# Performance work log

Measured on AMD Instinct MI355X. Metric: run time of the kernel, lower is better.

The kernel has to match this reference:

```python
import jax, jax.numpy as jnp
import numpy as np

N = 100000
E = 3200000
HEADS = 4
DH = 16  # per-head dim
IN = 300
OUT2 = 32
SLOPE = 0.2  # PyG GATConv leaky_relu negative slope


def setup_inputs() -> dict:
    key = jax.random.key(0)
    ks = jax.random.split(key, 10)
    x = jax.random.normal(ks[0], (N, IN), dtype=jnp.float32)
    edge_index = jax.random.randint(ks[1], (2, E), 0, N, dtype=jnp.int64)
    sec_order_edge_index = jax.random.randint(ks[2], (2, E), 0, N, dtype=jnp.int64)
    # GATConv(300, 16, heads=4) params
    W1 = jax.random.normal(ks[3], (IN, HEADS * DH), dtype=jnp.float32) * (1.0 / np.sqrt(IN))
    att_src = jax.random.normal(ks[4], (HEADS, DH), dtype=jnp.float32) * 0.1
    att_dst = jax.random.normal(ks[5], (HEADS, DH), dtype=jnp.float32) * 0.1
    b1 = jnp.zeros((HEADS * DH,), dtype=jnp.float32)
    # GCNConv(64, 32) params
    W2 = jax.random.normal(ks[6], (HEADS * DH, OUT2), dtype=jnp.float32) * (1.0 / np.sqrt(HEADS * DH))
    b2 = jnp.zeros((OUT2,), dtype=jnp.float32)
    return {"x": x, "W1": W1, "att_src": att_src, "att_dst": att_dst, "b1": b1,
            "W2": W2, "b2": b2, "edge_index": edge_index,
            "sec_order_edge_index": sec_order_edge_index}


def _add_self_loops(edge_index, n):
    loop = jnp.arange(n, dtype=edge_index.dtype)
    src = jnp.concatenate([edge_index[0], loop])
    dst = jnp.concatenate([edge_index[1], loop])
    return src, dst


def _gat(x, W1, att_src, att_dst, b1, edge_index):
    n = x.shape[0]
    src, dst = _add_self_loops(edge_index, n)
    h = (x @ W1).reshape(n, HEADS, DH)                    # [N,H,D]
    a_s = jnp.einsum('nhd,hd->nh', h, att_src)            # [N,H]
    a_d = jnp.einsum('nhd,hd->nh', h, att_dst)
    e = jax.nn.leaky_relu(a_s[src] + a_d[dst], SLOPE)     # [Et,H]
    # segment softmax over edges grouped by destination node
    m = jax.ops.segment_max(e, dst, num_segments=n)       # [N,H]
    ex = jnp.exp(e - m[dst])
    denom = jax.ops.segment_sum(ex, dst, num_segments=n)  # [N,H] (>0: self-loops)
    alpha = ex / denom[dst]                               # [Et,H]
    out = jax.ops.segment_sum(h[src] * alpha[:, :, None], dst, num_segments=n)
    return out.reshape(n, HEADS * DH) + b1


def _gcn(x, W2, b2, edge_index):
    n = x.shape[0]
    src, dst = _add_self_loops(edge_index, n)
    deg = jax.ops.segment_sum(jnp.ones_like(dst, dtype=x.dtype), dst, num_segments=n)
    dinv = jnp.where(deg > 0, jax.lax.rsqrt(deg), 0.0)
    norm = dinv[src] * dinv[dst]                          # [Et]
    h = x @ W2                                            # [N,32]
    out = jax.ops.segment_sum(h[src] * norm[:, None], dst, num_segments=n)
    return out + b2


def reference(x, W1, att_src, att_dst, b1, W2, b2, edge_index, sec_order_edge_index):
    x1 = jax.nn.relu(_gat(x, W1, att_src, att_dst, b1, edge_index))
    # F.dropout with training=False is identity (eval mode)
    return _gcn(x1, W2, b2, sec_order_edge_index)
```

## Files before the change

kernel.cpp:

```cpp
#include <hip/hip_runtime.h>
#include <hip/hip_fp16.h>

#define N_NODES 100000
#define N_EDGES 3200000
#define TOT_E   (N_EDGES + N_NODES)
#define HEADS   4
#define DH      16
#define IN_F    300
#define HID     64
#define OUT2    32
#define SLOPE   0.2f
#define NBK     512
#define GSZ     196
#define EBLK    4096
#define NBA     ((TOT_E + EBLK - 1) / EBLK)

typedef _Float16 f16x8 __attribute__((ext_vector_type(8)));
typedef float    f32x4 __attribute__((ext_vector_type(4)));

__global__ void k_wcvt(const float* __restrict__ W1, __half* __restrict__ BT16) {
    int idx = blockIdx.x * 256 + threadIdx.x;
    if (idx >= HID * 320) return;
    int n = idx / 320, k = idx - n * 320;
    BT16[idx] = (k < IN_F) ? __float2half(W1[(size_t)k * HID + n]) : __float2half(0.f);
}

#define G1_BM 128
#define G1_BK 64
#define G1_NS 5

__global__ __launch_bounds__(256) void k_gemm1(const float* __restrict__ x,
                                               const __half* __restrict__ BT16,
                                               const float* __restrict__ att_src,
                                               const float* __restrict__ att_dst,
                                               __half* __restrict__ h16,
                                               float* __restrict__ as_ad) {
    __shared__ _Float16 At[G1_BM][G1_BK];
    __shared__ _Float16 Bt[HID][G1_BK];
    const int t = threadIdx.x;
    const int lane = t & 63, w = t >> 6;
    const int lr = lane & 15, lg = lane >> 4;
    const int row0 = blockIdx.x * G1_BM;
    const int wrow = w * 32;

    int arow[4], auc[4];
    const float* axp[4];
#pragma unroll
    for (int m = 0; m < 4; m++) {
        int id = t + m * 256;
        arow[m] = id >> 3; auc[m] = id & 7;
        int gr = row0 + arow[m];
        gr = (gr < N_NODES) ? gr : (N_NODES - 1);
        axp[m] = x + (size_t)gr * IN_F + auc[m] * 8;
    }
    int bn[2], buc[2];
    const __half* bxp[2];
#pragma unroll
    for (int q = 0; q < 2; q++) {
        int id = t + q * 256;
        bn[q] = id >> 3; buc[q] = id & 7;
        bxp[q] = BT16 + bn[q] * (G1_BK * G1_NS) + buc[q] * 8;
    }

    float4 ar[4][2];
    uint4  br[2];

    auto loadS = [&](int kb) {
        if (kb + G1_BK <= IN_F) {
#pragma unroll
            for (int m = 0; m < 4; m++) {
                ar[m][0] = *(const float4*)(axp[m] + kb);
                ar[m][1] = *(const float4*)(axp[m] + kb + 4);
            }
        } else {
#pragma unroll
            for (int m = 0; m < 4; m++) {
                float v[8];
#pragma unroll
                for (int e = 0; e < 8; e++) {
                    int k = kb + auc[m] * 8 + e;
                    v[e] = (k < IN_F) ? axp[m][kb + e] : 0.f;
                }
                ar[m][0] = make_float4(v[0], v[1], v[2], v[3]);
                ar[m][1] = make_float4(v[4], v[5], v[6], v[7]);
            }
        }
#pragma unroll
        for (int q = 0; q < 2; q++) br[q] = *(const uint4*)(bxp[q] + kb);
    };

    auto writeS = [&]() {
#pragma unroll
        for (int m = 0; m < 4; m++) {
            f16x8 pk;
            pk[0] = (_Float16)ar[m][0].x; pk[1] = (_Float16)ar[m][0].y;
            pk[2] = (_Float16)ar[m][0].z; pk[3] = (_Float16)ar[m][0].w;
            pk[4] = (_Float16)ar[m][1].x; pk[5] = (_Float16)ar[m][1].y;
            pk[6] = (_Float16)ar[m][1].z; pk[7] = (_Float16)ar[m][1].w;
            *(f16x8*)&At[arow[m]][(auc[m] ^ (arow[m] & 7)) << 3] = pk;
        }
#pragma unroll
        for (int q = 0; q < 2; q++)
            *(uint4*)&Bt[bn[q]][(buc[q] ^ (bn[q] & 7)) << 3] = br[q];
    };

    f32x4 acc[2][4];
#pragma unroll
    for (int mt = 0; mt < 2; mt++)
#pragma unroll
        for (int nt = 0; nt < 4; nt++) acc[mt][nt] = (f32x4){0.f, 0.f, 0.f, 0.f};

    loadS(0);
    for (int s = 0; s < G1_NS; s++) {
        __syncthreads();
        writeS();
        if (s + 1 < G1_NS) loadS((s + 1) * G1_BK);
        __syncthreads();
#pragma unroll
        for (int ks = 0; ks < 2; ks++) {
            const int u = ks * 4 + lg;
            f16x8 af[2], bf[4];
#pragma unroll
            for (int mt = 0; mt < 2; mt++) {
                int r = wrow + mt * 16 + lr;
                af[mt] = *(const f16x8*)&At[r][(u ^ (r & 7)) << 3];
            }
#pragma unroll
            for (int nt = 0; nt < 4; nt++) {
                int n = nt * 16 + lr;
                bf[nt] = *(const f16x8*)&Bt[n][(u ^ (n & 7)) << 3];
            }
#pragma unroll
            for (int mt = 0; mt < 2; mt++)
#pragma unroll
                for (int nt = 0; nt < 4; nt++)
                    acc[mt][nt] = __builtin_amdgcn_mfma_f32_16x16x32_f16(
                        af[mt], bf[nt], acc[mt][nt], 0, 0, 0);
        }
    }

    float ws4[4], wd4[4];
#pragma unroll
    for (int nt = 0; nt < 4; nt++) {
        ws4[nt] = att_src[nt * DH + lr];
        wd4[nt] = att_dst[nt * DH + lr];
    }

#pragma unroll
    for (int mt = 0; mt < 2; mt++) {
#pragma unroll
        for (int rg = 0; rg < 4; rg++) {
            int gr = row0 + wrow + mt * 16 + lg * 4 + rg;
            float s_[4], d_[4];
#pragma unroll
            for (int nt = 0; nt < 4; nt++) {
                float v = (float)acc[mt][nt][rg];
                float vs = v * ws4[nt], vd = v * wd4[nt];
                vs += __shfl_xor(vs, 1, 64); vs += __shfl_xor(vs, 2, 64);
                vs += __shfl_xor(vs, 4, 64); vs += __shfl_xor(vs, 8, 64);
                vd += __shfl_xor(vd, 1, 64); vd += __shfl_xor(vd, 2, 64);
                vd += __shfl_xor(vd, 4, 64); vd += __shfl_xor(vd, 8, 64);
                s_[nt] = vs; d_[nt] = vd;
            }
            if (gr < N_NODES) {
#pragma unroll
                for (int nt = 0; nt < 4; nt++)
                    h16[(size_t)gr * HID + nt * 16 + lr] =
                        __float2half((float)acc[mt][nt][rg]);
                if (lr == 0) {
                    *(float4*)&as_ad[gr * 8] =
                        make_float4(s_[0], s_[1], s_[2], s_[3]);
                    *(float4*)&as_ad[gr * 8 + 4] =
                        make_float4(d_[0], d_[1], d_[2], d_[3]);
                }
            }
        }
    }
}

__global__ __launch_bounds__(512) void k_chist(const int* __restrict__ ei1,
                                               const int* __restrict__ ei2,
                                               int* __restrict__ ccnt) {
    __shared__ int hist[NBK];
    int b = blockIdx.x; const int* ei; int* cc;
    if (b < NBA) { ei = ei1; cc = ccnt; }
    else         { ei = ei2; cc = ccnt + NBK; b -= NBA; }
    int t = threadIdx.x;
    hist[t] = 0;
    __syncthreads();
    int e0 = b * EBLK;
#pragma unroll
    for (int i = 0; i < 8; i++) {
        int e = e0 + i * 512 + t;
        if (e < TOT_E) {
            int dst = (e < N_EDGES) ? ei[N_EDGES + e] : (e - N_EDGES);
            atomicAdd(&hist[(unsigned int)dst / GSZ], 1);
        }
    }
    __syncthreads();
    { int v = hist[t]; if (v) atomicAdd(&cc[t], v); }
}

__global__ __launch_bounds__(1024) void k_cscan(const int* __restrict__ ccnt,
                                                int* __restrict__ crp,
                                                int* __restrict__ ccur) {
    __shared__ int sc[1024];
    int t = threadIdx.x;
    int idx = t & (NBK - 1);
    int own = ccnt[t];
    sc[t] = own;
    __syncthreads();
    for (int off = 1; off < NBK; off <<= 1) {
        int v = (idx >= off) ? sc[t - off] : 0;
        __syncthreads();
        sc[t] += v;
        __syncthreads();
    }
    int ex = sc[t] - own;
    crp[t] = ex; ccur[t] = ex;
}

__global__ __launch_bounds__(512) void k_binA(const int* __restrict__ ei1,
                                              const int* __restrict__ ei2,
                                              int* __restrict__ ccur,
                                              unsigned int* __restrict__ tmp) {
    __shared__ int hist[NBK];
    __shared__ int base[NBK];
    int b = blockIdx.x; const int* ei; int loff;
    if (b < NBA) { ei = ei1; loff = 0; }
    else         { ei = ei2; loff = 1; b -= NBA; }
    int t = threadIdx.x;
    hist[t] = 0;
    __syncthreads();
    unsigned int pk[8]; int cb[8], rk[8];
    int e0 = b * EBLK;
#pragma unroll
    for (int i = 0; i < 8; i++) {
        int e = e0 + i * 512 + t;
        cb[i] = -1;
        if (e < TOT_E) {
            int src, dst;
            if (e < N_EDGES) { src = ei[e]; dst = ei[N_EDGES + e]; }
            else             { src = e - N_EDGES; dst = src; }
            unsigned int c   = (unsigned int)dst / GSZ;
            unsigned int dlo = (unsigned int)dst - c * GSZ;
            cb[i] = (int)c;
            pk[i] = (dlo << 17) | (unsigned int)src;
            rk[i] = atomicAdd(&hist[c], 1);
        }
    }
    __syncthreads();
    {
        int v = hist[t];
        base[t] = v ? atomicAdd(&ccur[loff * NBK + t], v) : 0;
    }
    __syncthreads();
    unsigned int* tp = tmp + (size_t)loff * TOT_E;
#pragma unroll
    for (int i = 0; i < 8; i++)
        if (cb[i] >= 0) tp[base[cb[i]] + rk[i]] = pk[i];
}

__global__ __launch_bounds__(256) void k_binB(const unsigned int* __restrict__ tmp,
                                              const int* __restrict__ crp,
                                              int* __restrict__ rowptr,
                                              int* __restrict__ srcs,
                                              float* __restrict__ dinv) {
    __shared__ int cnt[GSZ + 1];
    __shared__ int sc[256];
    __shared__ int cur[GSZ + 1];
    int blk = blockIdx.x;
    int l = blk >> 9, b = blk & (NBK - 1);
    int t = threadIdx.x;
    int nbeg = b * GSZ;
    int ncnt = min(GSZ, N_NODES - nbeg);
    const int* crpl = crp + l * NBK;
    int ebeg = crpl[b];
    int eend = (b < NBK - 1) ? crpl[b + 1] : TOT_E;
    const unsigned int* tp = tmp + (size_t)l * TOT_E;
    for (int i = t; i < GSZ + 1; i += 256) cnt[i] = 0;
    __syncthreads();
    for (int e = ebeg + t; e < eend; e += 256)
        atomicAdd(&cnt[tp[e] >> 17], 1);
    __syncthreads();
    sc[t] = (t < ncnt) ? cnt[t] : 0;
    __syncthreads();
    for (int off = 1; off < 256; off <<= 1) {
        int v = (t >= off) ? sc[t - off] : 0;
        __syncthreads();
        sc[t] += v;
        __syncthreads();
    }
    if (t < ncnt) {
        int c = cnt[t];
        int gpos = ebeg + sc[t] - c;
        rowptr[l * N_NODES + nbeg + t] = gpos;
        cur[t] = gpos;
        if (l == 1) dinv[nbeg + t] = rsqrtf((float)c);
    }
    __syncthreads();
    int* so = srcs + (size_t)l * TOT_E;
    for (int e = ebeg + t; e < eend; e += 256) {
        unsigned int p = tp[e];
        int pos = atomicAdd(&cur[p >> 17], 1);
        so[pos] = (int)(p & 0x1FFFF);
    }
}

__global__ __launch_bounds__(256) void k_gat(const __half* __restrict__ h16,
                                             const float* __restrict__ as_ad,
                                             const int* __restrict__ rowptr,
                                             const int* __restrict__ srcs,
                                             const float* __restrict__ b1,
                                             __half* __restrict__ x1h) {
    int w = (blockIdx.x * 256 + threadIdx.x) >> 6;
    if (w >= N_NODES) return;
    int lane = threadIdx.x & 63;
    int eidx = lane >> 3;
    int cl = lane & 7;
    int hd = cl >> 1;
    int c0 = cl * 8;
    float ad = as_ad[w * 8 + 4 + hd];
    int beg = rowptr[w];
    int end = (w == N_NODES - 1) ? TOT_E : rowptr[w + 1];
    float l = 0.f;
    float a0 = 0.f, a1 = 0.f, a2 = 0.f, a3 = 0.f;
    float a4 = 0.f, a5 = 0.f, a6 = 0.f, a7 = 0.f;
#pragma unroll 4
    for (int j = beg; j < end; j += 8) {
        int je = j + eidx;
        int s = __builtin_nontemporal_load(&srcs[min(je, end - 1)]);
        uint4 raw = *(const uint4*)&h16[(size_t)s * HID + c0];
        float e = as_ad[s * 8 + hd] + ad;
        e = fminf(fmaxf(e, SLOPE * e), 60.f);
        float p = (je < end) ? __expf(e) : 0.f;
        l += p;
        const __half2* hv = (const __half2*)&raw;
        float2 f0 = __half22float2(hv[0]);
        float2 f1 = __half22float2(hv[1]);
        float2 f2 = __half22float2(hv[2]);
        float2 f3 = __half22float2(hv[3]);
        a0 += p * f0.x; a1 += p * f0.y; a2 += p * f1.x; a3 += p * f1.y;
        a4 += p * f2.x; a5 += p * f2.y; a6 += p * f3.x; a7 += p * f3.y;
    }
    l  += __shfl_xor(l, 8, 64);  l  += __shfl_xor(l, 16, 64);  l  += __shfl_xor(l, 32, 64);
    a0 += __shfl_xor(a0, 8, 64); a0 += __shfl_xor(a0, 16, 64); a0 += __shfl_xor(a0, 32, 64);
    a1 += __shfl_xor(a1, 8, 64); a1 += __shfl_xor(a1, 16, 64); a1 += __shfl_xor(a1, 32, 64);
    a2 += __shfl_xor(a2, 8, 64); a2 += __shfl_xor(a2, 16, 64); a2 += __shfl_xor(a2, 32, 64);
    a3 += __shfl_xor(a3, 8, 64); a3 += __shfl_xor(a3, 16, 64); a3 += __shfl_xor(a3, 32, 64);
    a4 += __shfl_xor(a4, 8, 64); a4 += __shfl_xor(a4, 16, 64); a4 += __shfl_xor(a4, 32, 64);
    a5 += __shfl_xor(a5, 8, 64); a5 += __shfl_xor(a5, 16, 64); a5 += __shfl_xor(a5, 32, 64);
    a6 += __shfl_xor(a6, 8, 64); a6 += __shfl_xor(a6, 16, 64); a6 += __shfl_xor(a6, 32, 64);
    a7 += __shfl_xor(a7, 8, 64); a7 += __shfl_xor(a7, 16, 64); a7 += __shfl_xor(a7, 32, 64);
    if (eidx == 0) {
        float rl = 1.f / l;
        float4 b0 = *(const float4*)&b1[c0];
        float4 b4 = *(const float4*)&b1[c0 + 4];
        f16x8 o;
        o[0] = (_Float16)fmaxf(a0 * rl + b0.x, 0.f);
        o[1] = (_Float16)fmaxf(a1 * rl + b0.y, 0.f);
        o[2] = (_Float16)fmaxf(a2 * rl + b0.z, 0.f);
        o[3] = (_Float16)fmaxf(a3 * rl + b0.w, 0.f);
        o[4] = (_Float16)fmaxf(a4 * rl + b4.x, 0.f);
        o[5] = (_Float16)fmaxf(a5 * rl + b4.y, 0.f);
        o[6] = (_Float16)fmaxf(a6 * rl + b4.z, 0.f);
        o[7] = (_Float16)fmaxf(a7 * rl + b4.w, 0.f);
        *(f16x8*)&x1h[(size_t)w * HID + c0] = o;
    }
}

__global__ __launch_bounds__(256) void k_gemm2(const __half* __restrict__ x1h,
                                               const float* __restrict__ W2,
                                               const float* __restrict__ dinv,
                                               __half* __restrict__ h2s) {
    __shared__ float wl[HID * OUT2];
    __shared__ float xl[32][HID];
    int t = threadIdx.x;
    for (int i = t; i < HID * OUT2; i += 256) wl[i] = W2[i];
    int row0 = blockIdx.x * 32;
    {
        int rr = t >> 3, kk0 = (t & 7) * 8;
        uint4 raw = *(const uint4*)&x1h[(size_t)(row0 + rr) * HID + kk0];
        const __half2* hv = (const __half2*)&raw;
#pragma unroll
        for (int q = 0; q < 4; q++) {
            float2 f = __half22float2(hv[q]);
            xl[rr][kk0 + 2 * q] = f.x;
            xl[rr][kk0 + 2 * q + 1] = f.y;
        }
    }
    __syncthreads();
    int r0 = (t >> 5) * 4, c = t & 31;
    float ac0 = 0.f, ac1 = 0.f, ac2 = 0.f, ac3 = 0.f;
#pragma unroll 8
    for (int k = 0; k < HID; k++) {
        float wv = wl[k * OUT2 + c];
        ac0 += xl[r0 + 0][k] * wv;
        ac1 += xl[r0 + 1][k] * wv;
        ac2 += xl[r0 + 2][k] * wv;
        ac3 += xl[r0 + 3][k] * wv;
    }
    h2s[(size_t)(row0 + r0 + 0) * OUT2 + c] = __float2half(ac0 * dinv[row0 + r0 + 0]);
    h2s[(size_t)(row0 + r0 + 1) * OUT2 + c] = __float2half(ac1 * dinv[row0 + r0 + 1]);
    h2s[(size_t)(row0 + r0 + 2) * OUT2 + c] = __float2half(ac2 * dinv[row0 + r0 + 2]);
    h2s[(size_t)(row0 + r0 + 3) * OUT2 + c] = __float2half(ac3 * dinv[row0 + r0 + 3]);
}

__global__ __launch_bounds__(256) void k_gcn(const __half* __restrict__ h2s,
                                             const float* __restrict__ dinv,
                                             const int* __restrict__ rowptr,
                                             const int* __restrict__ srcs,
                                             const float* __restrict__ b2,
                                             float* __restrict__ out) {
    int w = (blockIdx.x * 256 + threadIdx.x) >> 6;
    if (w >= N_NODES) return;
    int lane = threadIdx.x & 63;
    int eidx = lane >> 2;
    int cq = lane & 3;
    int c0 = cq * 8;
    int beg = rowptr[w];
    int end = (w == N_NODES - 1) ? TOT_E : rowptr[w + 1];
    float a0 = 0.f, a1 = 0.f, a2 = 0.f, a3 = 0.f;
    float a4 = 0.f, a5 = 0.f, a6 = 0.f, a7 = 0.f;
#pragma unroll 4
    for (int j = beg; j < end; j += 16) {
        int je = j + eidx;
        int s = __builtin_nontemporal_load(&srcs[min(je, end - 1)]);
        uint4 raw = *(const uint4*)&h2s[(size_t)s * OUT2 + c0];
        if (je < end) {
            const __half2* hv = (const __half2*)&raw;
            float2 f0 = __half22float2(hv[0]);
            float2 f1 = __half22float2(hv[1]);
            float2 f2 = __half22float2(hv[2]);
            float2 f3 = __half22float2(hv[3]);
            a0 += f0.x; a1 += f0.y; a2 += f1.x; a3 += f1.y;
            a4 += f2.x; a5 += f2.y; a6 += f3.x; a7 += f3.y;
        }
    }
    a0 += __shfl_xor(a0, 4, 64); a0 += __shfl_xor(a0, 8, 64); a0 += __shfl_xor(a0, 16, 64); a0 += __shfl_xor(a0, 32, 64);
    a1 += __shfl_xor(a1, 4, 64); a1 += __shfl_xor(a1, 8, 64); a1 += __shfl_xor(a1, 16, 64); a1 += __shfl_xor(a1, 32, 64);
    a2 += __shfl_xor(a2, 4, 64); a2 += __shfl_xor(a2, 8, 64); a2 += __shfl_xor(a2, 16, 64); a2 += __shfl_xor(a2, 32, 64);
    a3 += __shfl_xor(a3, 4, 64); a3 += __shfl_xor(a3, 8, 64); a3 += __shfl_xor(a3, 16, 64); a3 += __shfl_xor(a3, 32, 64);
    a4 += __shfl_xor(a4, 4, 64); a4 += __shfl_xor(a4, 8, 64); a4 += __shfl_xor(a4, 16, 64); a4 += __shfl_xor(a4, 32, 64);
    a5 += __shfl_xor(a5, 4, 64); a5 += __shfl_xor(a5, 8, 64); a5 += __shfl_xor(a5, 16, 64); a5 += __shfl_xor(a5, 32, 64);
    a6 += __shfl_xor(a6, 4, 64); a6 += __shfl_xor(a6, 8, 64); a6 += __shfl_xor(a6, 16, 64); a6 += __shfl_xor(a6, 32, 64);
    a7 += __shfl_xor(a7, 4, 64); a7 += __shfl_xor(a7, 8, 64); a7 += __shfl_xor(a7, 16, 64); a7 += __shfl_xor(a7, 32, 64);
    if (eidx == 0) {
        float dv = dinv[w];
        float4 b0 = *(const float4*)&b2[c0];
        float4 b4 = *(const float4*)&b2[c0 + 4];
        float4 o0 = make_float4(a0 * dv + b0.x, a1 * dv + b0.y,
                                a2 * dv + b0.z, a3 * dv + b0.w);
        float4 o4 = make_float4(a4 * dv + b4.x, a5 * dv + b4.y,
                                a6 * dv + b4.z, a7 * dv + b4.w);
        *(float4*)&out[(size_t)w * OUT2 + c0] = o0;
        *(float4*)&out[(size_t)w * OUT2 + c0 + 4] = o4;
    }
}

static inline size_t align_up(size_t v, size_t a) { return (v + a - 1) & ~(a - 1); }

extern "C" void kernel_launch(void* const* d_in, const int* in_sizes, int n_in,
                              void* d_out, int out_size, void* d_ws, size_t ws_size,
                              hipStream_t stream) {
    const float* x       = (const float*)d_in[0];
    const float* W1      = (const float*)d_in[1];
    const float* att_src = (const float*)d_in[2];
    const float* att_dst = (const float*)d_in[3];
    const float* b1      = (const float*)d_in[4];
    const float* W2      = (const float*)d_in[5];
    const float* b2      = (const float*)d_in[6];
    const int*   ei1     = (const int*)d_in[7];
    const int*   ei2     = (const int*)d_in[8];
    float* out = (float*)d_out;

    char* p = (char*)d_ws;
    size_t off = 0;
    auto carve = [&](size_t bytes) { void* q = p + off; off = align_up(off + bytes, 256); return q; };
    __half* h16   = (__half*)carve((size_t)N_NODES * HID * 2);
    __half* x1h   = (__half*)carve((size_t)N_NODES * HID * 2);
    __half* h2s   = (__half*)carve((size_t)N_NODES * OUT2 * 2);
    float* as_ad  = (float*)carve((size_t)N_NODES * 8 * 4);
    float* dinv   = (float*)carve((size_t)N_NODES * 4);
    int* rowptr   = (int*)carve((size_t)2 * N_NODES * 4);
    int* srcs     = (int*)carve((size_t)2 * TOT_E * 4);
    unsigned int* tmp = (unsigned int*)carve((size_t)2 * TOT_E * 4);
    int* ccnt     = (int*)carve((size_t)2 * NBK * 4);
    int* crp      = (int*)carve((size_t)2 * NBK * 4);
    int* ccur     = (int*)carve((size_t)2 * NBK * 4);
    __half* BT16  = (__half*)carve((size_t)HID * 320 * 2);
    (void)ws_size; (void)in_sizes; (void)n_in; (void)out_size;

    hipMemsetAsync(ccnt, 0, (size_t)2 * NBK * 4, stream);

    k_wcvt<<<(HID * 320 + 255) / 256, 256, 0, stream>>>(W1, BT16);
    k_gemm1<<<(N_NODES + G1_BM - 1) / G1_BM, 256, 0, stream>>>(x, BT16, att_src, att_dst, h16, as_ad);

    k_chist<<<2 * NBA, 512, 0, stream>>>(ei1, ei2, ccnt);
    k_cscan<<<1, 1024, 0, stream>>>(ccnt, crp, ccur);
    k_binA<<<2 * NBA, 512, 0, stream>>>(ei1, ei2, ccur, tmp);
    k_binB<<<2 * NBK, 256, 0, stream>>>(tmp, crp, rowptr, srcs, dinv);

    k_gat<<<N_NODES / 4, 256, 0, stream>>>(h16, as_ad, rowptr, srcs, b1, x1h);

    k_gemm2<<<N_NODES / 32, 256, 0, stream>>>(x1h, W2, dinv, h2s);

    k_gcn<<<N_NODES / 4, 256, 0, stream>>>(h2s, dinv, rowptr + N_NODES, srcs + TOT_E, b2, out);
}
```

Baseline: 544.9 us.

## Halve GEMM1 row tile and stage outputs through LDS for coalesced stores

Shrinks the projection GEMM block tile from 128 to 64 rows, so each wave computes one 16-row MFMA tile and the grid has twice as many blocks. The epilogue now writes the accumulators to shared memory and reads them back per row and head, replacing the shuffle-based attention reductions and scattered 2-byte stores with vectorized 16-byte stores to h16. The attention logits are now computed from fp16-rounded values rather than fp32 accumulators, which slightly changes numerics. The smaller tile loads the weight matrix more times in total.

After: 543.5 us. About the same (-0.3%).

```diff
diff --git a/kernel.cpp b/kernel.cpp
--- a/kernel.cpp
+++ b/kernel.cpp
@@ -25,7 +25,7 @@
     BT16[idx] = (k < IN_F) ? __float2half(W1[(size_t)k * HID + n]) : __float2half(0.f);
 }
 
-#define G1_BM 128
+#define G1_BM 64
 #define G1_BK 64
 #define G1_NS 5
 
@@ -41,12 +41,12 @@
     const int lane = t & 63, w = t >> 6;
     const int lr = lane & 15, lg = lane >> 4;
     const int row0 = blockIdx.x * G1_BM;
-    const int wrow = w * 32;
-
-    int arow[4], auc[4];
-    const float* axp[4];
-#pragma unroll
-    for (int m = 0; m < 4; m++) {
+    const int wrow = w * 16;
+
+    int arow[2], auc[2];
+    const float* axp[2];
+#pragma unroll
+    for (int m = 0; m < 2; m++) {
         int id = t + m * 256;
         arow[m] = id >> 3; auc[m] = id & 7;
         int gr = row0 + arow[m];
@@ -62,19 +62,19 @@
         bxp[q] = BT16 + bn[q] * (G1_BK * G1_NS) + buc[q] * 8;
     }
 
-    float4 ar[4][2];
+    float4 ar[2][2];
     uint4  br[2];
 
     auto loadS = [&](int kb) {
         if (kb + G1_BK <= IN_F) {
 #pragma unroll
-            for (int m = 0; m < 4; m++) {
+            for (int m = 0; m < 2; m++) {
                 ar[m][0] = *(const float4*)(axp[m] + kb);
                 ar[m][1] = *(const float4*)(axp[m] + kb + 4);
             }
         } else {
 #pragma unroll
-            for (int m = 0; m < 4; m++) {
+            for (int m = 0; m < 2; m++) {
                 float v[8];
 #pragma unroll
                 for (int e = 0; e < 8; e++) {
@@ -91,7 +91,7 @@
 
     auto writeS = [&]() {
 #pragma unroll
-        for (int m = 0; m < 4; m++) {
+        for (int m = 0; m < 2; m++) {
             f16x8 pk;
             pk[0] = (_Float16)ar[m][0].x; pk[1] = (_Float16)ar[m][0].y;
             pk[2] = (_Float16)ar[m][0].z; pk[3] = (_Float16)ar[m][0].w;
@@ -104,11 +104,9 @@
             *(uint4*)&Bt[bn[q]][(buc[q] ^ (bn[q] & 7)) << 3] = br[q];
     };
 
-    f32x4 acc[2][4];
-#pragma unroll
-    for (int mt = 0; mt < 2; mt++)
-#pragma unroll
-        for (int nt = 0; nt < 4; nt++) acc[mt][nt] = (f32x4){0.f, 0.f, 0.f, 0.f};
+    f32x4 acc[4];
+#pragma unroll
+    for (int nt = 0; nt < 4; nt++) acc[nt] = (f32x4){0.f, 0.f, 0.f, 0.f};
 
     loadS(0);
     for (int s = 0; s < G1_NS; s++) {
@@ -119,11 +117,10 @@
 #pragma unroll
         for (int ks = 0; ks < 2; ks++) {
             const int u = ks * 4 + lg;
-            f16x8 af[2], bf[4];
-#pragma unroll
-            for (int mt = 0; mt < 2; mt++) {
-                int r = wrow + mt * 16 + lr;
-                af[mt] = *(const f16x8*)&At[r][(u ^ (r & 7)) << 3];
+            f16x8 af, bf[4];
+            {
+                int r = wrow + lr;
+                af = *(const f16x8*)&At[r][(u ^ (r & 7)) << 3];
             }
 #pragma unroll
             for (int nt = 0; nt < 4; nt++) {
@@ -131,49 +128,37 @@
                 bf[nt] = *(const f16x8*)&Bt[n][(u ^ (n & 7)) << 3];
             }
 #pragma unroll
-            for (int mt = 0; mt < 2; mt++)
-#pragma unroll
-                for (int nt = 0; nt < 4; nt++)
-                    acc[mt][nt] = __builtin_amdgcn_mfma_f32_16x16x32_f16(
-                        af[mt], bf[nt], acc[mt][nt], 0, 0, 0);
-        }
-    }
-
-    float ws4[4], wd4[4];
-#pragma unroll
-    for (int nt = 0; nt < 4; nt++) {
-        ws4[nt] = att_src[nt * DH + lr];
-        wd4[nt] = att_dst[nt * DH + lr];
-    }
-
-#pragma unroll
-    for (int mt = 0; mt < 2; mt++) {
-#pragma unroll
-        for (int rg = 0; rg < 4; rg++) {
-            int gr = row0 + wrow + mt * 16 + lg * 4 + rg;
-            float s_[4], d_[4];
-#pragma unroll
-            for (int nt = 0; nt < 4; nt++) {
-                float v = (float)acc[mt][nt][rg];
-                float vs = v * ws4[nt], vd = v * wd4[nt];
-                vs += __shfl_xor(vs, 1, 64); vs += __shfl_xor(vs, 2, 64);
-                vs += __shfl_xor(vs, 4, 64); vs += __shfl_xor(vs, 8, 64);
-                vd += __shfl_xor(vd, 1, 64); vd += __shfl_xor(vd, 2, 64);
-                vd += __shfl_xor(vd, 4, 64); vd += __shfl_xor(vd, 8, 64);
-                s_[nt] = vs; d_[nt] = vd;
-            }
-            if (gr < N_NODES) {
-#pragma unroll
-                for (int nt = 0; nt < 4; nt++)
-                    h16[(size_t)gr * HID + nt * 16 + lr] =
-                        __float2half((float)acc[mt][nt][rg]);
-                if (lr == 0) {
-                    *(float4*)&as_ad[gr * 8] =
-                        make_float4(s_[0], s_[1], s_[2], s_[3]);
-                    *(float4*)&as_ad[gr * 8 + 4] =
-                        make_float4(d_[0], d_[1], d_[2], d_[3]);
-                }
-            }
+            for (int nt = 0; nt < 4; nt++)
+                acc[nt] = __builtin_amdgcn_mfma_f32_16x16x32_f16(
+                    af, bf[nt], acc[nt], 0, 0, 0);
+        }
+    }
+
+    __syncthreads();
+#pragma unroll
+    for (int nt = 0; nt < 4; nt++)
+#pragma unroll
+        for (int rg = 0; rg < 4; rg++)
+            At[wrow + lg * 4 + rg][nt * DH + lr] = (_Float16)acc[nt][rg];
+    __syncthreads();
+
+    {
+        int row = t >> 2, hd = t & 3;
+        int gr = row0 + row;
+        f16x8 p0 = *(const f16x8*)&At[row][hd * DH];
+        f16x8 p1 = *(const f16x8*)&At[row][hd * DH + 8];
+        float s = 0.f, d = 0.f;
+#pragma unroll
+        for (int k = 0; k < 8; k++) {
+            float v0 = (float)p0[k], v1 = (float)p1[k];
+            s += v0 * att_src[hd * DH + k] + v1 * att_src[hd * DH + 8 + k];
+            d += v0 * att_dst[hd * DH + k] + v1 * att_dst[hd * DH + 8 + k];
+        }
+        if (gr < N_NODES) {
+            *(f16x8*)&h16[(size_t)gr * HID + hd * DH] = p0;
+            *(f16x8*)&h16[(size_t)gr * HID + hd * DH + 8] = p1;
+            as_ad[gr * 8 + hd] = s;
+            as_ad[gr * 8 + 4 + hd] = d;
         }
     }
 }
```
